# Performance work log

Measured on AMD Instinct MI355X. Metric: run time of the kernel, lower is better.

Reference implementation:

```python
import jax, jax.numpy as jnp
import numpy as np

B, N_PER, E_PER = 32, 2048, 4096          # graphs, nodes/graph, edges/graph
NN, NE = B * N_PER, B * E_PER              # 65536 nodes, 131072 edges
F_IN, EMB, H, OUT, VOCAB = 32, 32, 128, 64, 10000


def _glorot(k, shape):
    lim = float(np.sqrt(6.0 / (shape[0] + shape[-1])))
    return jax.random.uniform(k, shape, jnp.float32, -lim, lim)


def setup_inputs() -> dict:
    key = jax.random.key(0)
    ks = jax.random.split(key, 20)
    x = jax.random.normal(ks[0], (NN, F_IN), jnp.float32)
    node_index = jax.random.randint(ks[1], (NN,), 0, VOCAB)
    # intra-graph edges, nodes sorted by graph -> edge batch is sorted too
    off = jnp.repeat(jnp.arange(B) * N_PER, E_PER)
    src = jax.random.randint(ks[2], (NE,), 0, N_PER) + off
    dst = jax.random.randint(ks[3], (NE,), 0, N_PER) + off
    edge_index = jnp.stack([src, dst])
    d_in = F_IN + EMB
    return dict(
        x=x, node_index=node_index, edge_index=edge_index,
        emb=jax.random.normal(ks[4], (VOCAB, EMB), jnp.float32),
        W1=_glorot(ks[5], (d_in, H)), a1s=_glorot(ks[6], (H,)), a1d=_glorot(ks[7], (H,)), b1=jnp.zeros((H,), jnp.float32),
        W2=_glorot(ks[8], (H, H)),   a2s=_glorot(ks[9], (H,)), a2d=_glorot(ks[10], (H,)), b2=jnp.zeros((H,), jnp.float32),
        W3=_glorot(ks[11], (H, H)),  a3s=_glorot(ks[12], (H,)), a3d=_glorot(ks[13], (H,)), b3=jnp.zeros((H,), jnp.float32),
        fcW=_glorot(ks[14], (2 * H, H)), fcb=jnp.zeros((H,), jnp.float32),
        Wz=_glorot(ks[15], (H + OUT, OUT)), bz=jnp.zeros((OUT,), jnp.float32),
        Wr=_glorot(ks[16], (H + OUT, OUT)), br=jnp.zeros((OUT,), jnp.float32),
        Wh=_glorot(ks[17], (H + OUT, OUT)), bh=jnp.zeros((OUT,), jnp.float32),
    )


def _gat(h_in, W, a_s, a_d, b, src, dst):
    # single-head GATConv with self-loops already appended to (src, dst)
    h = h_in @ W                                              # [NN, H]
    e = jax.nn.leaky_relu((h @ a_s)[src] + (h @ a_d)[dst], 0.2)  # [E']
    m = jax.ops.segment_max(e, dst, num_segments=NN)
    ex = jnp.exp(e - m[dst])
    s = jax.ops.segment_sum(ex, dst, num_segments=NN)
    alpha = ex / s[dst]
    return jax.ops.segment_sum(h[src] * alpha[:, None], dst, num_segments=NN) + b


def reference(x, node_index, edge_index, emb, W1, a1s, a1d, b1, W2, a2s, a2d, b2,
              W3, a3s, a3d, b3, fcW, fcb, Wz, bz, Wr, br, Wh, bh):
    gelu = lambda v: jax.nn.gelu(v, approximate=False)  # torch F.gelu default = erf
    h = jnp.concatenate([x, emb[node_index]], axis=1)   # [NN, F_IN+EMB]
    loops = jnp.arange(NN)
    src = jnp.concatenate([edge_index[0], loops])
    dst = jnp.concatenate([edge_index[1], loops])
    h = gelu(_gat(h, W1, a1s, a1d, b1, src, dst))
    h = gelu(_gat(h, W2, a2s, a2d, b2, src, dst))
    h = gelu(_gat(h, W3, a3s, a3d, b3, src, dst))
    # per-edge features (original edges, no self-loops)
    ef = jnp.concatenate([h[edge_index[0]], h[edge_index[1]]], axis=-1)  # [NE, 2H]
    ef = gelu(ef @ fcW + fcb)                                            # [NE, H]
    # equal-size graphs, edges sorted by graph -> construct_tensor == reshape, mask all-ones
    gru_in = ef.reshape(B, E_PER, H).transpose(1, 0, 2)                  # [T, B, H]

    def step(hid, xt):
        c = jnp.concatenate([xt, hid], axis=1)
        z = jax.nn.sigmoid(c @ Wz + bz)
        r = jax.nn.sigmoid(c @ Wr + br)
        cr = jnp.concatenate([xt, r * hid], axis=1)
        ht = jax.nn.leaky_relu(cr @ Wh + bh, 0.01)
        return (1 - z) * hid + z * ht, None

    hid, _ = jax.lax.scan(step, jnp.zeros((B, OUT), ef.dtype), gru_in)
    # predict_graph=True with all-ones mask -> prediction at last timestep == final hidden
    return hid
```

## Files before the change

kernel.cpp:

```cpp
#include <hip/hip_runtime.h>
#include <hip/hip_bf16.h>
#include <math.h>

#define NN_ 65536
#define NE_ 131072
#define B_  32
#define T_  4096
#define D_  8

typedef __fp16 f16x2 __attribute__((ext_vector_type(2)));
typedef unsigned int u32;

__device__ __forceinline__ float gelu_f(float x){
    return 0.5f*x*(1.0f + erff(x*0.70710678118654752f));
}

__device__ __forceinline__ unsigned enc_f(float f){
    unsigned b = __float_as_uint(f);
    return (b & 0x80000000u) ? ~b : (b | 0x80000000u);
}
__device__ __forceinline__ float dec_f(unsigned u){
    return (u & 0x80000000u) ? __uint_as_float(u ^ 0x80000000u) : __uint_as_float(~u);
}

__device__ __forceinline__ int rdlane_i(int v, int l){
    return __builtin_amdgcn_readlane(v, l);
}
__device__ __forceinline__ int h2i(f16x2 h){ union{int i; f16x2 h;} u; u.h=h; return u.i; }
__device__ __forceinline__ f16x2 i2h(int i){ union{int i; f16x2 h;} u; u.i=i; return u.h; }

__device__ __forceinline__ float dot2(f16x2 a, f16x2 b, float c){
#if __has_builtin(__builtin_amdgcn_fdot2)
    return __builtin_amdgcn_fdot2(a, b, c, false);
#else
    return c + (float)a.x*(float)b.x + (float)a.y*(float)b.y;
#endif
}

__device__ __forceinline__ void gload_lds4(const float* g, float* l, int lane){
#if __has_builtin(__builtin_amdgcn_global_load_lds)
    __builtin_amdgcn_global_load_lds((const __attribute__((address_space(1))) u32*)g,
                                     (__attribute__((address_space(3))) u32*)l, 4, 0, 0);
#else
    l[lane] = *g;
#endif
}

__global__ void k_zero(float* p, int n){
    int i = blockIdx.x*blockDim.x + threadIdx.x;
    int stride = gridDim.x*blockDim.x;
    for(; i<n; i+=stride) p[i] = 0.f;
}

__global__ void k_embed(const float* __restrict__ x, const int* __restrict__ nidx,
                        const float* __restrict__ emb, float* __restrict__ h64){
    int gid = blockIdx.x*256 + threadIdx.x;
    int n = gid >> 6, c = gid & 63;
    float v = (c < 32) ? x[(size_t)n*32 + c] : emb[(size_t)nidx[n]*32 + (c-32)];
    h64[gid] = v;
}

template<int K>
__global__ void k_gemm_node(const float* __restrict__ A, const float* __restrict__ W,
                            float* __restrict__ C){
    int lane = threadIdx.x & 63;
    int wy = threadIdx.x >> 6;
    int r0 = blockIdx.x*16 + wy*4;
    const float* a0 = A + (size_t)r0*K;
    float acc0[4] = {0,0,0,0}, acc1[4] = {0,0,0,0};
    #pragma unroll 4
    for(int k=0;k<K;k+=4){
        float4 av[4];
        #pragma unroll
        for(int i=0;i<4;i++) av[i] = *(const float4*)(a0 + (size_t)i*K + k);
        #pragma unroll
        for(int kk=0;kk<4;kk++){
            float w0 = W[(size_t)(k+kk)*128 + lane];
            float w1 = W[(size_t)(k+kk)*128 + 64 + lane];
            #pragma unroll
            for(int i=0;i<4;i++){
                float a = ((const float*)&av[i])[kk];
                acc0[i] += a*w0;
                acc1[i] += a*w1;
            }
        }
    }
    #pragma unroll
    for(int i=0;i<4;i++){
        C[(size_t)(r0+i)*128 + lane]      = acc0[i];
        C[(size_t)(r0+i)*128 + 64 + lane] = acc1[i];
    }
}

__global__ void k_rowdots(const float* __restrict__ hW, const float* __restrict__ as_,
                          const float* __restrict__ ad_, float* __restrict__ ssrc,
                          float* __restrict__ sdst){
    int lane = threadIdx.x & 63;
    int row = blockIdx.x*4 + (threadIdx.x >> 6);
    const float* hp = hW + (size_t)row*128;
    float h0 = hp[lane], h1 = hp[lane+64];
    float d0 = h0*as_[lane] + h1*as_[lane+64];
    float d1 = h0*ad_[lane] + h1*ad_[lane+64];
    #pragma unroll
    for(int off=32; off; off>>=1){
        d0 += __shfl_xor(d0, off);
        d1 += __shfl_xor(d1, off);
    }
    if(lane==0){ ssrc[row] = d0; sdst[row] = d1; }
}

__global__ void k_edge1(const int* __restrict__ src, const int* __restrict__ dst,
                        const float* __restrict__ ssrc, const float* __restrict__ sdst,
                        float* __restrict__ ebuf, unsigned* __restrict__ menc){
    int e = blockIdx.x*256 + threadIdx.x;
    int s, d;
    if(e < NE_){ s = src[e]; d = dst[e]; } else { s = d = e - NE_; }
    float v = ssrc[s] + sdst[d];
    v = (v > 0.f) ? v : 0.2f*v;
    ebuf[e] = v;
    atomicMax(&menc[d], enc_f(v));
}

__global__ void k_edge2(const int* __restrict__ dst, const unsigned* __restrict__ menc,
                        float* __restrict__ ebuf, float* __restrict__ ssum){
    int e = blockIdx.x*256 + threadIdx.x;
    int d = (e < NE_) ? dst[e] : (e - NE_);
    float m = dec_f(menc[d]);
    float ex = __expf(ebuf[e] - m);
    ebuf[e] = ex;
    atomicAdd(&ssum[d], ex);
}

__global__ void __launch_bounds__(256) k_edge3_lds(
        const int* __restrict__ src, const int* __restrict__ dst,
        const float* __restrict__ ebuf, const float* __restrict__ ssum,
        const float* __restrict__ hW, const float* __restrict__ bias,
        float* __restrict__ hAgg){
    __shared__ float agg[2048][8];
    int g  = blockIdx.x;
    int c0 = blockIdx.y << 3;
    int t  = threadIdx.x;
    int cc = t & 7;
    int elane = t >> 3;

    for(int idx = t; idx < 2048*8; idx += 256)
        ((float*)agg)[idx] = 0.f;
    __syncthreads();

    const int gbase_e = g << 12;
    const int gbase_n = g << 11;
    for(int i = 0; i < 192; i++){
        int eg = i*32 + elane;
        int s, dloc; float a;
        if(eg < 4096){
            int e = gbase_e + eg;
            s    = src[e];
            int d = dst[e];
            dloc = d - gbase_n;
            a    = ebuf[e] / ssum[d];
        } else {
            int nl = eg - 4096;
            s    = gbase_n + nl;
            dloc = nl;
            a    = ebuf[NE_ + gbase_n + nl] / ssum[gbase_n + nl];
        }
        float v = hW[(size_t)s*128 + c0 + cc] * a;
        atomicAdd(&agg[dloc][cc], v);
    }
    __syncthreads();

    for(int idx = t; idx < 2048*8; idx += 256){
        int nl = idx >> 3;
        int ch = c0 + (idx & 7);
        hAgg[((size_t)(gbase_n + nl))*128 + ch] = gelu_f(agg[nl][idx & 7] + bias[ch]);
    }
}

__global__ void k_ef_x3(const float* __restrict__ h3, const int* __restrict__ src,
                        const int* __restrict__ dst, const float* __restrict__ fcW,
                        const float* __restrict__ fcb,
                        const float* __restrict__ Wz, const float* __restrict__ Wr,
                        const float* __restrict__ Wh, const float* __restrict__ bz,
                        const float* __restrict__ br, const float* __restrict__ bh,
                        float* __restrict__ X3){
    __shared__ float efs[16][128];
    int lane = threadIdx.x & 63;
    int wy = threadIdx.x >> 6;
    int e0 = blockIdx.x*16 + wy*4;

    {
        float acc0[4] = {0,0,0,0}, acc1[4] = {0,0,0,0};
        #pragma unroll
        for(int half=0; half<2; half++){
            const float* rowp[4];
            #pragma unroll
            for(int i=0;i<4;i++){
                int n = (half==0) ? src[e0+i] : dst[e0+i];
                rowp[i] = h3 + (size_t)n*128;
            }
            #pragma unroll 2
            for(int k=0;k<128;k+=4){
                float4 av[4];
                #pragma unroll
                for(int i=0;i<4;i++) av[i] = *(const float4*)(rowp[i] + k);
                #pragma unroll
                for(int kk=0;kk<4;kk++){
                    int kw = half*128 + k + kk;
                    float w0 = fcW[(size_t)kw*128 + lane];
                    float w1 = fcW[(size_t)kw*128 + 64 + lane];
                    #pragma unroll
                    for(int i=0;i<4;i++){
                        float a = ((const float*)&av[i])[kk];
                        acc0[i] += a*w0;
                        acc1[i] += a*w1;
                    }
                }
            }
        }
        float b0 = fcb[lane], b1 = fcb[64+lane];
        #pragma unroll
        for(int i=0;i<4;i++){
            efs[wy*4+i][lane]      = gelu_f(acc0[i] + b0);
            efs[wy*4+i][64 + lane] = gelu_f(acc1[i] + b1);
        }
    }
    __syncthreads();
    {
        float accz[4] = {0,0,0,0}, accr[4] = {0,0,0,0}, acch[4] = {0,0,0,0};
        #pragma unroll 2
        for(int k=0;k<128;k+=4){
            #pragma unroll
            for(int kk=0;kk<4;kk++){
                float w0 = Wz[(size_t)(k+kk)*64 + lane];
                float w1 = Wr[(size_t)(k+kk)*64 + lane];
                float w2 = Wh[(size_t)(k+kk)*64 + lane];
                #pragma unroll
                for(int i=0;i<4;i++){
                    float a = efs[wy*4+i][k+kk];
                    accz[i] += a*w0;
                    accr[i] += a*w1;
                    acch[i] += a*w2;
                }
            }
        }
        float b0 = bz[lane], b1 = br[lane], b2 = bh[lane];
        #pragma unroll
        for(int i=0;i<4;i++){
            int e = e0 + i;
            int bb = e >> 12;
            int t  = e & 4095;
            float* o = X3 + ((size_t)t*32 + bb)*192;
            o[lane]       = accz[i] + b0;
            o[64 + lane]  = accr[i] + b1;
            o[128 + lane] = acch[i] + b2;
        }
    }
}

__global__ void __launch_bounds__(256) k_gru(const float* __restrict__ X3,
                       const float* __restrict__ Wz, const float* __restrict__ Wr,
                       const float* __restrict__ Wh, float* __restrict__ out){
    __shared__ float  ring[D_][192];
    __shared__ float2 P1[4][64];
    __shared__ float  P2[4][64];
    int b = blockIdx.x;
    int j = threadIdx.x & 63;
    int w = __builtin_amdgcn_readfirstlane(threadIdx.x >> 6);
    int kbase = w << 4;
    int odd = j & 1;

    f16x2 wzp[8], wrp[8], whp[8];
    #pragma unroll
    for(int i=0;i<8;i++){
        int r0 = 128 + kbase + 2*i;
        wzp[i] = __builtin_amdgcn_cvt_pkrtz(Wz[(size_t)r0*64 + j], Wz[(size_t)(r0+1)*64 + j]);
        wrp[i] = __builtin_amdgcn_cvt_pkrtz(Wr[(size_t)r0*64 + j], Wr[(size_t)(r0+1)*64 + j]);
        whp[i] = __builtin_amdgcn_cvt_pkrtz(Wh[(size_t)r0*64 + j], Wh[(size_t)(r0+1)*64 + j]);
    }

    if(w == 0){
        for(int s=0;s<D_;s++){
            const float* gp = X3 + ((size_t)s*32 + b)*192 + j;
            gload_lds4(gp,       &ring[s][0],   j);
            gload_lds4(gp + 64,  &ring[s][64],  j);
            gload_lds4(gp + 128, &ring[s][128], j);
        }
        asm volatile("s_waitcnt vmcnt(21)" ::: "memory");
        __builtin_amdgcn_sched_barrier(0);
    }
    __builtin_amdgcn_s_barrier();

    float h = 0.f;
    for(int step=0; step<T_; step++){
        int sl = step & (D_-1);
        float xz = ring[sl][j], xr = ring[sl][64+j], xh = ring[sl][128+j];

        float hn = __shfl_xor(h, 1);
        int hp = h2i(__builtin_amdgcn_cvt_pkrtz(odd ? hn : h, odd ? h : hn));

        float az0=0.f, az1=0.f, ar0=0.f, ar1=0.f;
        #pragma unroll
        for(int i=0;i<8;i+=2){
            f16x2 h0 = i2h(rdlane_i(hp, kbase + 2*i));
            f16x2 h1 = i2h(rdlane_i(hp, kbase + 2*i + 2));
            az0 = dot2(h0, wzp[i],   az0); ar0 = dot2(h0, wrp[i],   ar0);
            az1 = dot2(h1, wzp[i+1], az1); ar1 = dot2(h1, wrp[i+1], ar1);
        }
        P1[w][j] = make_float2(az0+az1, ar0+ar1);
        asm volatile("s_waitcnt lgkmcnt(0)" ::: "memory");
        __builtin_amdgcn_s_barrier();

        if(w == 0){
            int ps = (step + D_ < T_) ? (step + D_) : (T_-1);
            const float* gp = X3 + ((size_t)ps*32 + b)*192 + j;
            gload_lds4(gp,       &ring[sl][0],   j);
            gload_lds4(gp + 64,  &ring[sl][64],  j);
            gload_lds4(gp + 128, &ring[sl][128], j);
        }

        float2 q0 = P1[0][j], q1 = P1[1][j], q2 = P1[2][j], q3 = P1[3][j];
        float sz = xz + ((q0.x+q1.x)+(q2.x+q3.x));
        float sr = xr + ((q0.y+q1.y)+(q2.y+q3.y));
        float z = __builtin_amdgcn_rcpf(1.f + __expf(-sz));
        float r = __builtin_amdgcn_rcpf(1.f + __expf(-sr));
        float rh = r*h;

        float rn = __shfl_xor(rh, 1);
        int rp = h2i(__builtin_amdgcn_cvt_pkrtz(odd ? rn : rh, odd ? rh : rn));

        float ah0=0.f, ah1=0.f;
        #pragma unroll
        for(int i=0;i<8;i+=2){
            f16x2 r0 = i2h(rdlane_i(rp, kbase + 2*i));
            f16x2 r1 = i2h(rdlane_i(rp, kbase + 2*i + 2));
            ah0 = dot2(r0, whp[i],   ah0);
            ah1 = dot2(r1, whp[i+1], ah1);
        }
        P2[w][j] = ah0 + ah1;
        if(w == 0){
            asm volatile("s_waitcnt vmcnt(21)" ::: "memory");
        }
        asm volatile("s_waitcnt lgkmcnt(0)" ::: "memory");
        __builtin_amdgcn_s_barrier();

        float s2 = xh + ((P2[0][j]+P2[1][j]) + (P2[2][j]+P2[3][j]));
        float ht = fmaxf(s2, 0.01f*s2);
        h = fmaf(z, ht - h, h);
    }
    if(w == 0) out[(size_t)b*64 + j] = h;
}

extern "C" void kernel_launch(void* const* d_in, const int* in_sizes, int n_in,
                              void* d_out, int out_size, void* d_ws, size_t ws_size,
                              hipStream_t stream) {
    const float* x    = (const float*)d_in[0];
    const int*   nidx = (const int*)d_in[1];
    const int*   src  = (const int*)d_in[2];
    const int*   dst  = src + NE_;
    const float* emb  = (const float*)d_in[3];
    const float* W1 = (const float*)d_in[4];
    const float* a1s = (const float*)d_in[5];
    const float* a1d = (const float*)d_in[6];
    const float* b1 = (const float*)d_in[7];
    const float* W2 = (const float*)d_in[8];
    const float* a2s = (const float*)d_in[9];
    const float* a2d = (const float*)d_in[10];
    const float* b2 = (const float*)d_in[11];
    const float* W3 = (const float*)d_in[12];
    const float* a3s = (const float*)d_in[13];
    const float* a3d = (const float*)d_in[14];
    const float* b3 = (const float*)d_in[15];
    const float* fcW = (const float*)d_in[16];
    const float* fcb = (const float*)d_in[17];
    const float* Wz = (const float*)d_in[18];
    const float* bz = (const float*)d_in[19];
    const float* Wr = (const float*)d_in[20];
    const float* br = (const float*)d_in[21];
    const float* Wh = (const float*)d_in[22];
    const float* bh = (const float*)d_in[23];
    float* out = (float*)d_out;

    float* ws = (float*)d_ws;
    float* hAgg = ws;
    float* X3   = hAgg + (size_t)NN_*128;
    float* bufA = X3;
    float* h64  = bufA + (size_t)NN_*128;
    float* ssrc = h64  + (size_t)NN_*64;
    float* sdst = ssrc + NN_;
    float* ssum = sdst + NN_;
    unsigned* menc = (unsigned*)(ssum + NN_);
    float* ebuf = (float*)menc + NN_;

    const int EP = NE_ + NN_;

    k_embed<<<NN_*64/256, 256, 0, stream>>>(x, nidx, emb, h64);

    const float* Ws[3]  = {W1, W2, W3};
    const float* as_[3] = {a1s, a2s, a3s};
    const float* ad_[3] = {a1d, a2d, a3d};
    const float* bs[3]  = {b1, b2, b3};

    for(int l=0; l<3; l++){
        if(l == 0)
            k_gemm_node<64><<<NN_/16, 256, 0, stream>>>(h64, Ws[l], bufA);
        else
            k_gemm_node<128><<<NN_/16, 256, 0, stream>>>(hAgg, Ws[l], bufA);
        k_zero<<<512, 256, 0, stream>>>(ssum, 2*NN_);
        k_rowdots<<<NN_/4, 256, 0, stream>>>(bufA, as_[l], ad_[l], ssrc, sdst);
        k_edge1<<<EP/256, 256, 0, stream>>>(src, dst, ssrc, sdst, ebuf, menc);
        k_edge2<<<EP/256, 256, 0, stream>>>(dst, menc, ebuf, ssum);
        k_edge3_lds<<<dim3(B_, 16), 256, 0, stream>>>(src, dst, ebuf, ssum, bufA, bs[l], hAgg);
    }

    k_ef_x3<<<NE_/16, 256, 0, stream>>>(hAgg, src, dst, fcW, fcb,
                                        Wz, Wr, Wh, bz, br, bh, X3);
    k_gru<<<B_, 256, 0, stream>>>(X3, Wz, Wr, Wh, out);
}
```

Baseline: 3.846 ms.

## Restructure GRU kernel to two waves with gate-per-wave split and fold zeroing

The sequential GRU recurrence kernel moves from four waves, each holding a K-slice of all three weight matrices, to two waves. Wave 0 computes the z gate and wave 1 the r gate over the full K=64, and both compute the candidate redundantly. The hidden state is shared as fp16 through LDS vector reads, replacing readlane broadcasts and the cross-wave partial-sum reductions. This aims to shorten the per-step critical path of the 4096-step serial loop. Separately, zeroing of ssum/menc is folded into the rowdots kernel to drop one launch per layer. The cost is more registers per thread and more redundant compute per wave.

```diff
diff --git a/kernel.cpp b/kernel.cpp
--- a/kernel.cpp
+++ b/kernel.cpp
@@ -23,9 +23,6 @@
     return (u & 0x80000000u) ? __uint_as_float(u ^ 0x80000000u) : __uint_as_float(~u);
 }
 
-__device__ __forceinline__ int rdlane_i(int v, int l){
-    return __builtin_amdgcn_readlane(v, l);
-}
 __device__ __forceinline__ int h2i(f16x2 h){ union{int i; f16x2 h;} u; u.h=h; return u.i; }
 __device__ __forceinline__ f16x2 i2h(int i){ union{int i; f16x2 h;} u; u.i=i; return u.h; }
 
@@ -44,12 +41,6 @@
 #else
     l[lane] = *g;
 #endif
-}
-
-__global__ void k_zero(float* p, int n){
-    int i = blockIdx.x*blockDim.x + threadIdx.x;
-    int stride = gridDim.x*blockDim.x;
-    for(; i<n; i+=stride) p[i] = 0.f;
 }
 
 __global__ void k_embed(const float* __restrict__ x, const int* __restrict__ nidx,
@@ -94,7 +85,8 @@
 
 __global__ void k_rowdots(const float* __restrict__ hW, const float* __restrict__ as_,
                           const float* __restrict__ ad_, float* __restrict__ ssrc,
-                          float* __restrict__ sdst){
+                          float* __restrict__ sdst, float* __restrict__ ssum,
+                          unsigned* __restrict__ menc){
     int lane = threadIdx.x & 63;
     int row = blockIdx.x*4 + (threadIdx.x >> 6);
     const float* hp = hW + (size_t)row*128;
@@ -106,7 +98,10 @@
         d0 += __shfl_xor(d0, off);
         d1 += __shfl_xor(d1, off);
     }
-    if(lane==0){ ssrc[row] = d0; sdst[row] = d1; }
+    if(lane==0){
+        ssrc[row] = d0; sdst[row] = d1;
+        ssum[row] = 0.f; menc[row] = 0u;
+    }
 }
 
 __global__ void k_edge1(const int* __restrict__ src, const int* __restrict__ dst,
@@ -257,26 +252,27 @@
     }
 }
 
-__global__ void __launch_bounds__(256) k_gru(const float* __restrict__ X3,
+__global__ void __launch_bounds__(128) k_gru(const float* __restrict__ X3,
                        const float* __restrict__ Wz, const float* __restrict__ Wr,
                        const float* __restrict__ Wh, float* __restrict__ out){
     __shared__ float  ring[D_][192];
-    __shared__ float2 P1[4][64];
-    __shared__ float  P2[4][64];
+    __shared__ float  Zs[2][64];
+    __shared__ __align__(16) unsigned short RHs[2][64];
+    __shared__ __align__(16) unsigned short Hs[2][64];
     int b = blockIdx.x;
     int j = threadIdx.x & 63;
     int w = __builtin_amdgcn_readfirstlane(threadIdx.x >> 6);
-    int kbase = w << 4;
-    int odd = j & 1;
-
-    f16x2 wzp[8], wrp[8], whp[8];
+
+    const float* Wg = (w == 0) ? Wz : Wr;
+    f16x2 wgp[32], whp[32];
     #pragma unroll
-    for(int i=0;i<8;i++){
-        int r0 = 128 + kbase + 2*i;
-        wzp[i] = __builtin_amdgcn_cvt_pkrtz(Wz[(size_t)r0*64 + j], Wz[(size_t)(r0+1)*64 + j]);
-        wrp[i] = __builtin_amdgcn_cvt_pkrtz(Wr[(size_t)r0*64 + j], Wr[(size_t)(r0+1)*64 + j]);
+    for(int i=0;i<32;i++){
+        int r0 = 128 + 2*i;
+        wgp[i] = __builtin_amdgcn_cvt_pkrtz(Wg[(size_t)r0*64 + j], Wg[(size_t)(r0+1)*64 + j]);
         whp[i] = __builtin_amdgcn_cvt_pkrtz(Wh[(size_t)r0*64 + j], Wh[(size_t)(r0+1)*64 + j]);
     }
+
+    Hs[w][j] = 0;
 
     if(w == 0){
         for(int s=0;s<D_;s++){
@@ -288,25 +284,38 @@
         asm volatile("s_waitcnt vmcnt(21)" ::: "memory");
         __builtin_amdgcn_sched_barrier(0);
     }
+    asm volatile("s_waitcnt lgkmcnt(0)" ::: "memory");
     __builtin_amdgcn_s_barrier();
 
     float h = 0.f;
+    const int gate_off = w << 6;
     for(int step=0; step<T_; step++){
         int sl = step & (D_-1);
-        float xz = ring[sl][j], xr = ring[sl][64+j], xh = ring[sl][128+j];
-
-        float hn = __shfl_xor(h, 1);
-        int hp = h2i(__builtin_amdgcn_cvt_pkrtz(odd ? hn : h, odd ? h : hn));
-
-        float az0=0.f, az1=0.f, ar0=0.f, ar1=0.f;
-        #pragma unroll
-        for(int i=0;i<8;i+=2){
-            f16x2 h0 = i2h(rdlane_i(hp, kbase + 2*i));
-            f16x2 h1 = i2h(rdlane_i(hp, kbase + 2*i + 2));
-            az0 = dot2(h0, wzp[i],   az0); ar0 = dot2(h0, wrp[i],   ar0);
-            az1 = dot2(h1, wzp[i+1], az1); ar1 = dot2(h1, wrp[i+1], ar1);
-        }
-        P1[w][j] = make_float2(az0+az1, ar0+ar1);
+        int p  = step & 1;
+        float xg = ring[sl][gate_off + j];
+        float xh = ring[sl][128 + j];
+
+        const uint4* hp4 = (const uint4*)&Hs[w][0];
+        float a0 = xg, a1 = 0.f, a2 = 0.f, a3 = 0.f;
+        #pragma unroll
+        for(int m=0;m<8;m++){
+            uint4 u = hp4[m];
+            a0 = dot2(i2h((int)u.x), wgp[4*m],   a0);
+            a1 = dot2(i2h((int)u.y), wgp[4*m+1], a1);
+            a2 = dot2(i2h((int)u.z), wgp[4*m+2], a2);
+            a3 = dot2(i2h((int)u.w), wgp[4*m+3], a3);
+        }
+        float sg = (a0+a1)+(a2+a3);
+        float g  = __builtin_amdgcn_rcpf(1.f + __expf(-sg));
+        if(w == 0){
+            Zs[p][j] = g;
+        } else {
+            float rh = g * h;
+            RHs[p][j] = (unsigned short)(h2i(__builtin_amdgcn_cvt_pkrtz(rh, rh)) & 0xffff);
+        }
+        if(w == 0){
+            asm volatile("s_waitcnt vmcnt(18)" ::: "memory");
+        }
         asm volatile("s_waitcnt lgkmcnt(0)" ::: "memory");
         __builtin_amdgcn_s_barrier();
 
@@ -318,34 +327,21 @@
             gload_lds4(gp + 128, &ring[sl][128], j);
         }
 
-        float2 q0 = P1[0][j], q1 = P1[1][j], q2 = P1[2][j], q3 = P1[3][j];
-        float sz = xz + ((q0.x+q1.x)+(q2.x+q3.x));
-        float sr = xr + ((q0.y+q1.y)+(q2.y+q3.y));
-        float z = __builtin_amdgcn_rcpf(1.f + __expf(-sz));
-        float r = __builtin_amdgcn_rcpf(1.f + __expf(-sr));
-        float rh = r*h;
-
-        float rn = __shfl_xor(rh, 1);
-        int rp = h2i(__builtin_amdgcn_cvt_pkrtz(odd ? rn : rh, odd ? rh : rn));
-
-        float ah0=0.f, ah1=0.f;
-        #pragma unroll
-        for(int i=0;i<8;i+=2){
-            f16x2 r0 = i2h(rdlane_i(rp, kbase + 2*i));
-            f16x2 r1 = i2h(rdlane_i(rp, kbase + 2*i + 2));
-            ah0 = dot2(r0, whp[i],   ah0);
-            ah1 = dot2(r1, whp[i+1], ah1);
-        }
-        P2[w][j] = ah0 + ah1;
-        if(w == 0){
-            asm volatile("s_waitcnt vmcnt(21)" ::: "memory");
-        }
-        asm volatile("s_waitcnt lgkmcnt(0)" ::: "memory");
-        __builtin_amdgcn_s_barrier();
-
-        float s2 = xh + ((P2[0][j]+P2[1][j]) + (P2[2][j]+P2[3][j]));
+        const uint4* rp4 = (const uint4*)&RHs[p][0];
+        float c0 = xh, c1 = 0.f, c2 = 0.f, c3 = 0.f;
+        #pragma unroll
+        for(int m=0;m<8;m++){
+            uint4 u = rp4[m];
+            c0 = dot2(i2h((int)u.x), whp[4*m],   c0);
+            c1 = dot2(i2h((int)u.y), whp[4*m+1], c1);
+            c2 = dot2(i2h((int)u.z), whp[4*m+2], c2);
+            c3 = dot2(i2h((int)u.w), whp[4*m+3], c3);
+        }
+        float s2 = (c0+c1)+(c2+c3);
         float ht = fmaxf(s2, 0.01f*s2);
+        float z  = (w == 0) ? g : Zs[p][j];
         h = fmaf(z, ht - h, h);
+        Hs[w][j] = (unsigned short)(h2i(__builtin_amdgcn_cvt_pkrtz(h, h)) & 0xffff);
     }
     if(w == 0) out[(size_t)b*64 + j] = h;
 }
@@ -405,8 +401,7 @@
             k_gemm_node<64><<<NN_/16, 256, 0, stream>>>(h64, Ws[l], bufA);
         else
             k_gemm_node<128><<<NN_/16, 256, 0, stream>>>(hAgg, Ws[l], bufA);
-        k_zero<<<512, 256, 0, stream>>>(ssum, 2*NN_);
-        k_rowdots<<<NN_/4, 256, 0, stream>>>(bufA, as_[l], ad_[l], ssrc, sdst);
+        k_rowdots<<<NN_/4, 256, 0, stream>>>(bufA, as_[l], ad_[l], ssrc, sdst, ssum, menc);
         k_edge1<<<EP/256, 256, 0, stream>>>(src, dst, ssrc, sdst, ebuf, menc);
         k_edge2<<<EP/256, 256, 0, stream>>>(dst, menc, ebuf, ssum);
         k_edge3_lds<<<dim3(B_, 16), 256, 0, stream>>>(src, dst, ebuf, ssum, bufA, bs[l], hAgg);
@@ -414,5 +409,5 @@
 
     k_ef_x3<<<NE_/16, 256, 0, stream>>>(hAgg, src, dst, fcW, fcb,
                                         Wz, Wr, Wh, bz, br, bh, X3);
-    k_gru<<<B_, 256, 0, stream>>>(X3, Wz, Wr, Wh, out);
-}
+    k_gru<<<B_, 128, 0, stream>>>(X3, Wz, Wr, Wh, out);
+}
```

After: 3.405 ms. 1.13x faster.
